# Kernel tuning notes

Measured on AMD Instinct MI355X. Metric: run time of the kernel, lower is better.

The kernel has to match this reference:

```python
import jax, jax.numpy as jnp
import numpy as np

EPS = 1e-12


def setup_inputs() -> dict:
    key = jax.random.key(0)
    k1, k2 = jax.random.split(key)
    ide_feats = jax.random.normal(k1, (4096, 256), dtype=jnp.float32)
    u_feats = jax.random.normal(k2, (16384, 256), dtype=jnp.float32)
    return {"ide_feats": ide_feats, "u_feats": u_feats}


def reference(ide_feats, u_feats):
    # euclidean_dist: sqrt(sum((x_i - y_j)^2) + eps) -> [N, M]
    # computed via the GEMM expansion to avoid the [N, M, D] intermediate
    x2 = jnp.sum(ide_feats * ide_feats, axis=-1)[:, None]   # [N, 1]
    y2 = jnp.sum(u_feats * u_feats, axis=-1)[None, :]       # [1, M]
    xy = jnp.einsum('nd,md->nm', ide_feats, u_feats)        # [N, M]
    d2 = jnp.maximum(x2 + y2 - 2.0 * xy, 0.0)
    dists = jnp.sqrt(d2 + EPS)                              # [N, M]
    d = jnp.mean(dists, axis=-1)                            # [N]
    # dist_loss: sum_{i,j} sqrt((d_i - d_j)^2 + eps)
    diff = d[:, None] - d[None, :]                          # [N, N]
    loss = jnp.sum(jnp.sqrt(diff * diff + EPS))
    return loss
```

## Files before the change

### kernel.cpp

```cpp
#include <hip/hip_runtime.h>
#include <hip/hip_bf16.h>
#include <cstdint>

#define N_IDE 4096
#define M_U   16384
#define D_DIM 256
#define EPSF  1e-12f
#define INV_M (1.0f / 16384.0f)

typedef _Float16 f16x8 __attribute__((ext_vector_type(8)));
typedef float    f32x4 __attribute__((ext_vector_type(4)));

__device__ __forceinline__ void gll16(const void* g, void* l) {
  __builtin_amdgcn_global_load_lds(
      (const __attribute__((address_space(1))) void*)(uintptr_t)g,
      (__attribute__((address_space(3))) void*)(uint32_t)(uintptr_t)l,
      16, 0, 0);
}

__device__ __forceinline__ unsigned short f2h_bits(float f) {
  _Float16 h = (_Float16)f;
  return __builtin_bit_cast(unsigned short, h);
}

__global__ __launch_bounds__(256) void k_conv(const float* __restrict__ ide,
                                              const float* __restrict__ u,
                                              unsigned short* __restrict__ Ah,
                                              unsigned short* __restrict__ Bh,
                                              float* __restrict__ x2,
                                              float* __restrict__ y2,
                                              float* __restrict__ out0) {
  if (blockIdx.x == 0 && threadIdx.x == 0) *out0 = 0.f;
  int gw = (blockIdx.x * 256 + threadIdx.x) >> 6;
  int l  = threadIdx.x & 63;
  const float4* src;
  float* nrm;
  ushort4* dst;
  if (gw < N_IDE) {
    src = (const float4*)(ide + (size_t)gw * D_DIM);
    nrm = x2 + gw;
    dst = (ushort4*)(Ah + (size_t)gw * D_DIM) + l;
  } else {
    int c = gw - N_IDE;
    src = (const float4*)(u + (size_t)c * D_DIM);
    nrm = y2 + c;
    size_t chunk = ((size_t)(c >> 4) * 8 + (l >> 3)) * 64 + ((l >> 1) & 3) * 16 + (c & 15);
    dst = (ushort4*)(Bh + chunk * 8 + (l & 1) * 4);
  }
  float4 v = src[l];
  float s = v.x * v.x + v.y * v.y + v.z * v.z + v.w * v.w;
  ushort4 o;
  o.x = f2h_bits(v.x); o.y = f2h_bits(v.y);
  o.z = f2h_bits(v.z); o.w = f2h_bits(v.w);
  *dst = o;
#pragma unroll
  for (int m = 1; m <= 32; m <<= 1) s += __shfl_xor(s, m, 64);
  if (l == 0) *nrm = s;
}

__global__ __launch_bounds__(512, 2) void k_gemm(const unsigned short* __restrict__ Ah,
                                                 const unsigned short* __restrict__ Bh,
                                                 const float* __restrict__ x2,
                                                 const float* __restrict__ y2,
                                                 float* __restrict__ partial) {
  __shared__ __align__(16) unsigned short sA[128 * 256];
  __shared__ float rowacc[4][128];

  const int t    = threadIdx.x;
  const int w    = t >> 6;
  const int l    = t & 63;
  const int wm   = w >> 2, wn = w & 3;
  const int lrow = l & 15;
  const int lhi  = l >> 4;
  const int bx   = blockIdx.x;
  const int by   = blockIdx.y;

  rowacc[t >> 7][t & 127] = 0.f;

#pragma unroll
  for (int i = 0; i < 8; ++i)
    gll16(Ah + (size_t)(by * 128 + w * 16 + lrow) * D_DIM + (i * 4 + lhi) * 8,
          sA + (size_t)(i * 512 + w * 64) * 8);

  const unsigned short* Bbase = Bh + (size_t)(wn * 4) * 8 * 512 + (size_t)l * 8;
  auto loadB = [&](f16x8* buf, int s) {
    const int cgi = (s >> 3) * 8 + bx;
    const int kt  = s & 7;
    const unsigned short* p = Bbase + ((size_t)cgi * 16 * 8 + kt) * 512;
#pragma unroll
    for (int ni = 0; ni < 4; ++ni)
      buf[ni] = *(const f16x8*)(p + (size_t)ni * 8 * 512);
  };

  float4 x2v[4];
#pragma unroll
  for (int mi = 0; mi < 4; ++mi)
    x2v[mi] = *(const float4*)&x2[by * 128 + wm * 64 + mi * 16 + lhi * 4];

  f16x8 bf0[4], bf1[4];
  loadB(bf0, 0);

  __syncthreads();

  for (int cg = 0; cg < 8; ++cg) {
    const int cgi = cg * 8 + bx;

    f32x4 acc[4][4];
#pragma unroll
    for (int mi = 0; mi < 4; ++mi)
#pragma unroll
      for (int ni = 0; ni < 4; ++ni)
        acc[mi][ni] = (f32x4){0.f, 0.f, 0.f, 0.f};

    auto step = [&](int kt, const f16x8* bf) {
      f16x8 af[4];
#pragma unroll
      for (int mi = 0; mi < 4; ++mi)
        af[mi] = *(const f16x8*)(sA + (size_t)((kt * 8 + wm * 4 + mi) * 64 + l) * 8);
#pragma unroll
      for (int mi = 0; mi < 4; ++mi)
#pragma unroll
        for (int ni = 0; ni < 4; ++ni)
          acc[mi][ni] = __builtin_amdgcn_mfma_f32_16x16x32_f16(af[mi], bf[ni],
                                                               acc[mi][ni], 0, 0, 0);
    };

#pragma unroll
    for (int ktp = 0; ktp < 4; ++ktp) {
      const int s = cg * 8 + ktp * 2;
      loadB(bf1, s + 1);
      step(ktp * 2, bf0);
      loadB(bf0, (s + 2 < 64) ? s + 2 : 63);
      step(ktp * 2 + 1, bf1);
    }

    float yv[4];
#pragma unroll
    for (int ni = 0; ni < 4; ++ni)
      yv[ni] = y2[cgi * 256 + wn * 64 + ni * 16 + lrow];

#pragma unroll
    for (int mi = 0; mi < 4; ++mi) {
      float xr[4] = {x2v[mi].x, x2v[mi].y, x2v[mi].z, x2v[mi].w};
#pragma unroll
      for (int rr = 0; rr < 4; ++rr) {
        float ssum = 0.f;
#pragma unroll
        for (int ni = 0; ni < 4; ++ni) {
          float d2 = xr[rr] + yv[ni] - 2.0f * acc[mi][ni][rr];
          d2 = fmaxf(d2, 0.0f);
          ssum += __builtin_amdgcn_sqrtf(d2 + EPSF);
        }
        ssum += __shfl_xor(ssum, 1, 64);
        ssum += __shfl_xor(ssum, 2, 64);
        ssum += __shfl_xor(ssum, 4, 64);
        ssum += __shfl_xor(ssum, 8, 64);
        if (lrow == 0)
          rowacc[wn][wm * 64 + mi * 16 + lhi * 4 + rr] += ssum;
      }
    }
  }

  __syncthreads();
  if (t < 128)
    partial[(size_t)bx * N_IDE + by * 128 + t] =
        rowacc[0][t] + rowacc[1][t] + rowacc[2][t] + rowacc[3][t];
}

__global__ __launch_bounds__(256) void k_loss(const float* __restrict__ partial,
                                              float* __restrict__ out) {
  __shared__ float sd[N_IDE];
  __shared__ float wsum[4];
  int t = threadIdx.x;
  for (int k = t; k < N_IDE; k += 256) {
    float s = 0.f;
#pragma unroll
    for (int b = 0; b < 8; ++b) s += partial[(size_t)b * N_IDE + k];
    sd[k] = s;
  }
  __syncthreads();
  int tid = blockIdx.x * 256 + t;
  int i   = tid >> 4;
  int jl  = tid & 15;
  float di = sd[i];
  float s  = 0.f;
  for (int k = 0; k < 256; ++k) {
    float diff = (di - sd[jl + k * 16]) * INV_M;
    s += __builtin_amdgcn_sqrtf(diff * diff + EPSF);
  }
#pragma unroll
  for (int m = 1; m <= 32; m <<= 1) s += __shfl_xor(s, m, 64);
  if ((t & 63) == 0) wsum[t >> 6] = s;
  __syncthreads();
  if (t == 0) atomicAdd(out, wsum[0] + wsum[1] + wsum[2] + wsum[3]);
}

extern "C" void kernel_launch(void* const* d_in, const int* in_sizes, int n_in,
                              void* d_out, int out_size, void* d_ws, size_t ws_size,
                              hipStream_t stream) {
  (void)in_sizes; (void)n_in; (void)out_size; (void)ws_size;
  const float* ide = (const float*)d_in[0];
  const float* u   = (const float*)d_in[1];
  float* out = (float*)d_out;

  char* ws = (char*)d_ws;
  size_t off = 0;
  unsigned short* Ah = (unsigned short*)(ws + off); off += (size_t)N_IDE * D_DIM * 2;
  unsigned short* Bh = (unsigned short*)(ws + off); off += (size_t)M_U  * D_DIM * 2;
  float* x2      = (float*)(ws + off); off += (size_t)N_IDE * 4;
  float* y2      = (float*)(ws + off); off += (size_t)M_U * 4;
  float* partial = (float*)(ws + off); off += (size_t)8 * N_IDE * 4;

  k_conv<<<(N_IDE + M_U) / 4, 256, 0, stream>>>(ide, u, Ah, Bh, x2, y2, out);
  k_gemm<<<dim3(8, 32), 512, 0, stream>>>(Ah, Bh, x2, y2, partial);
  k_loss<<<256, 256, 0, stream>>>(partial, out);
}
```

Measured before the change: 147.9 us.

## Widen per-wave GEMM tile to full 128 rows and coalesce B conversion via LDS

The GEMM warp layout changes from a 2x4 split (64 rows x 64 cols per wave) to each of 8 waves covering all 128 rows x 64 columns. Each block now handles a contiguous 2048-column range, so every B fragment is loaded once per wave and reused across 8 A fragments instead of 4, halving global B traffic per MFMA. The conversion kernel now processes 16 rows per block and stages the fp16 B tile in shared memory so the swizzled layout is written with coalesced stores. In exchange, accumulator register pressure doubles (8x4 f32x4 per wave), which may cause spills or lower occupancy under launch_bounds(512,2).

```diff
diff --git a/kernel.cpp b/kernel.cpp
--- a/kernel.cpp
+++ b/kernel.cpp
@@ -30,32 +30,65 @@
                                               float* __restrict__ x2,
                                               float* __restrict__ y2,
                                               float* __restrict__ out0) {
-  if (blockIdx.x == 0 && threadIdx.x == 0) *out0 = 0.f;
-  int gw = (blockIdx.x * 256 + threadIdx.x) >> 6;
-  int l  = threadIdx.x & 63;
-  const float4* src;
-  float* nrm;
-  ushort4* dst;
-  if (gw < N_IDE) {
-    src = (const float4*)(ide + (size_t)gw * D_DIM);
-    nrm = x2 + gw;
-    dst = (ushort4*)(Ah + (size_t)gw * D_DIM) + l;
+  __shared__ unsigned short sh[16 * 260];
+  const int bid = blockIdx.x;
+  const int t   = threadIdx.x;
+  if (bid == 0 && t == 0) *out0 = 0.f;
+  const int rl = t >> 4;
+  const int kq = t & 15;
+  const int k0 = kq * 16;
+
+  if (bid < 256) {
+    const int row = bid * 16 + rl;
+    const float4* src = (const float4*)(ide + (size_t)row * D_DIM + k0);
+    float s = 0.f;
+    uint4 pk[2];
+    unsigned int* pw = (unsigned int*)pk;
+#pragma unroll
+    for (int q = 0; q < 4; ++q) {
+      float4 v = src[q];
+      s += v.x * v.x + v.y * v.y + v.z * v.z + v.w * v.w;
+      pw[q * 2 + 0] = (unsigned int)f2h_bits(v.x) | ((unsigned int)f2h_bits(v.y) << 16);
+      pw[q * 2 + 1] = (unsigned int)f2h_bits(v.z) | ((unsigned int)f2h_bits(v.w) << 16);
+    }
+    uint4* dst = (uint4*)(Ah + (size_t)row * D_DIM + k0);
+    dst[0] = pk[0];
+    dst[1] = pk[1];
+    s += __shfl_xor(s, 1, 64); s += __shfl_xor(s, 2, 64);
+    s += __shfl_xor(s, 4, 64); s += __shfl_xor(s, 8, 64);
+    if (kq == 0) x2[row] = s;
   } else {
-    int c = gw - N_IDE;
-    src = (const float4*)(u + (size_t)c * D_DIM);
-    nrm = y2 + c;
-    size_t chunk = ((size_t)(c >> 4) * 8 + (l >> 3)) * 64 + ((l >> 1) & 3) * 16 + (c & 15);
-    dst = (ushort4*)(Bh + chunk * 8 + (l & 1) * 4);
-  }
-  float4 v = src[l];
-  float s = v.x * v.x + v.y * v.y + v.z * v.z + v.w * v.w;
-  ushort4 o;
-  o.x = f2h_bits(v.x); o.y = f2h_bits(v.y);
-  o.z = f2h_bits(v.z); o.w = f2h_bits(v.w);
-  *dst = o;
-#pragma unroll
-  for (int m = 1; m <= 32; m <<= 1) s += __shfl_xor(s, m, 64);
-  if (l == 0) *nrm = s;
+    const int g   = bid - 256;
+    const int row = g * 16 + rl;
+    const float4* src = (const float4*)(u + (size_t)row * D_DIM + k0);
+    float s = 0.f;
+#pragma unroll
+    for (int q = 0; q < 4; ++q) {
+      float4 v = src[q];
+      s += v.x * v.x + v.y * v.y + v.z * v.z + v.w * v.w;
+      ushort4 o;
+      o.x = f2h_bits(v.x); o.y = f2h_bits(v.y);
+      o.z = f2h_bits(v.z); o.w = f2h_bits(v.w);
+      *(ushort4*)&sh[rl * 260 + k0 + q * 4] = o;
+    }
+    s += __shfl_xor(s, 1, 64); s += __shfl_xor(s, 2, 64);
+    s += __shfl_xor(s, 4, 64); s += __shfl_xor(s, 8, 64);
+    if (kq == 0) y2[row] = s;
+    __syncthreads();
+#pragma unroll
+    for (int j = 0; j < 4; ++j) {
+      int q_idx = j * 256 + t;
+      int uofs  = q_idx * 4;
+      int c_id  = uofs >> 3;
+      int h     = (uofs >> 2) & 1;
+      int kt    = c_id >> 6;
+      int lane  = c_id & 63;
+      int colw  = lane & 15;
+      int kk    = kt * 32 + ((lane >> 4) & 3) * 8 + h * 4;
+      ushort4 vv = *(const ushort4*)&sh[colw * 260 + kk];
+      *(ushort4*)(Bh + (size_t)g * 4096 + uofs) = vv;
+    }
+  }
 }
 
 __global__ __launch_bounds__(512, 2) void k_gemm(const unsigned short* __restrict__ Ah,
@@ -64,84 +97,76 @@
                                                  const float* __restrict__ y2,
                                                  float* __restrict__ partial) {
   __shared__ __align__(16) unsigned short sA[128 * 256];
-  __shared__ float rowacc[4][128];
+  __shared__ float rowacc[8][128];
 
   const int t    = threadIdx.x;
   const int w    = t >> 6;
   const int l    = t & 63;
-  const int wm   = w >> 2, wn = w & 3;
   const int lrow = l & 15;
   const int lhi  = l >> 4;
   const int bx   = blockIdx.x;
   const int by   = blockIdx.y;
 
-  rowacc[t >> 7][t & 127] = 0.f;
+  ((float*)rowacc)[t]       = 0.f;
+  ((float*)rowacc)[t + 512] = 0.f;
 
 #pragma unroll
   for (int i = 0; i < 8; ++i)
     gll16(Ah + (size_t)(by * 128 + w * 16 + lrow) * D_DIM + (i * 4 + lhi) * 8,
           sA + (size_t)(i * 512 + w * 64) * 8);
 
-  const unsigned short* Bbase = Bh + (size_t)(wn * 4) * 8 * 512 + (size_t)l * 8;
+  const unsigned short* Bb = Bh + (size_t)l * 8;
   auto loadB = [&](f16x8* buf, int s) {
-    const int cgi = (s >> 3) * 8 + bx;
-    const int kt  = s & 7;
-    const unsigned short* p = Bbase + ((size_t)cgi * 16 * 8 + kt) * 512;
+    const int p  = s >> 3;
+    const int kt = s & 7;
+    const size_t gb = ((size_t)(bx * 128 + p * 32 + w * 4) * 8 + kt) * 512;
 #pragma unroll
     for (int ni = 0; ni < 4; ++ni)
-      buf[ni] = *(const f16x8*)(p + (size_t)ni * 8 * 512);
+      buf[ni] = *(const f16x8*)(Bb + gb + (size_t)ni * 8 * 512);
   };
-
-  float4 x2v[4];
-#pragma unroll
-  for (int mi = 0; mi < 4; ++mi)
-    x2v[mi] = *(const float4*)&x2[by * 128 + wm * 64 + mi * 16 + lhi * 4];
 
   f16x8 bf0[4], bf1[4];
   loadB(bf0, 0);
 
   __syncthreads();
 
-  for (int cg = 0; cg < 8; ++cg) {
-    const int cgi = cg * 8 + bx;
-
-    f32x4 acc[4][4];
-#pragma unroll
-    for (int mi = 0; mi < 4; ++mi)
+  for (int p = 0; p < 4; ++p) {
+    f32x4 acc[8][4];
+#pragma unroll
+    for (int mi = 0; mi < 8; ++mi)
 #pragma unroll
       for (int ni = 0; ni < 4; ++ni)
         acc[mi][ni] = (f32x4){0.f, 0.f, 0.f, 0.f};
 
     auto step = [&](int kt, const f16x8* bf) {
-      f16x8 af[4];
-#pragma unroll
-      for (int mi = 0; mi < 4; ++mi)
-        af[mi] = *(const f16x8*)(sA + (size_t)((kt * 8 + wm * 4 + mi) * 64 + l) * 8);
-#pragma unroll
-      for (int mi = 0; mi < 4; ++mi)
+#pragma unroll
+      for (int mi = 0; mi < 8; ++mi) {
+        f16x8 a = *(const f16x8*)(sA + (size_t)((kt * 8 + mi) * 64 + l) * 8);
 #pragma unroll
         for (int ni = 0; ni < 4; ++ni)
-          acc[mi][ni] = __builtin_amdgcn_mfma_f32_16x16x32_f16(af[mi], bf[ni],
+          acc[mi][ni] = __builtin_amdgcn_mfma_f32_16x16x32_f16(a, bf[ni],
                                                                acc[mi][ni], 0, 0, 0);
+      }
     };
 
 #pragma unroll
     for (int ktp = 0; ktp < 4; ++ktp) {
-      const int s = cg * 8 + ktp * 2;
+      const int s = p * 8 + ktp * 2;
       loadB(bf1, s + 1);
       step(ktp * 2, bf0);
-      loadB(bf0, (s + 2 < 64) ? s + 2 : 63);
+      loadB(bf0, (s + 2 < 32) ? s + 2 : 31);
       step(ktp * 2 + 1, bf1);
     }
 
     float yv[4];
 #pragma unroll
     for (int ni = 0; ni < 4; ++ni)
-      yv[ni] = y2[cgi * 256 + wn * 64 + ni * 16 + lrow];
-
-#pragma unroll
-    for (int mi = 0; mi < 4; ++mi) {
-      float xr[4] = {x2v[mi].x, x2v[mi].y, x2v[mi].z, x2v[mi].w};
+      yv[ni] = y2[bx * 2048 + p * 512 + w * 64 + ni * 16 + lrow];
+
+#pragma unroll
+    for (int mi = 0; mi < 8; ++mi) {
+      float4 xv = *(const float4*)&x2[by * 128 + mi * 16 + lhi * 4];
+      float xr[4] = {xv.x, xv.y, xv.z, xv.w};
 #pragma unroll
       for (int rr = 0; rr < 4; ++rr) {
         float ssum = 0.f;
@@ -156,15 +181,18 @@
         ssum += __shfl_xor(ssum, 4, 64);
         ssum += __shfl_xor(ssum, 8, 64);
         if (lrow == 0)
-          rowacc[wn][wm * 64 + mi * 16 + lhi * 4 + rr] += ssum;
+          rowacc[w][mi * 16 + lhi * 4 + rr] += ssum;
       }
     }
   }
 
   __syncthreads();
-  if (t < 128)
-    partial[(size_t)bx * N_IDE + by * 128 + t] =
-        rowacc[0][t] + rowacc[1][t] + rowacc[2][t] + rowacc[3][t];
+  if (t < 128) {
+    float s = 0.f;
+#pragma unroll
+    for (int w8 = 0; w8 < 8; ++w8) s += rowacc[w8][t];
+    partial[(size_t)bx * N_IDE + by * 128 + t] = s;
+  }
 }
 
 __global__ __launch_bounds__(256) void k_loss(const float* __restrict__ partial,
@@ -211,7 +239,7 @@
   float* y2      = (float*)(ws + off); off += (size_t)M_U * 4;
   float* partial = (float*)(ws + off); off += (size_t)8 * N_IDE * 4;
 
-  k_conv<<<(N_IDE + M_U) / 4, 256, 0, stream>>>(ide, u, Ah, Bh, x2, y2, out);
+  k_conv<<<256 + 1024, 256, 0, stream>>>(ide, u, Ah, Bh, x2, y2, out);
   k_gemm<<<dim3(8, 32), 512, 0, stream>>>(Ah, Bh, x2, y2, partial);
   k_loss<<<256, 256, 0, stream>>>(partial, out);
 }
```

Measured after the change: 200.8 us. 1.36x slower.
